# Kernel optimization log

Measured on AMD Instinct MI355X. Metric: run time of the kernel, lower is better.

Reference implementation:

```python
import jax, jax.numpy as jnp
import numpy as np

B, C, H, W = 8, 256, 64, 64
C8 = C // 8


def setup_inputs() -> dict:
    key = jax.random.key(0)
    ks = jax.random.split(key, 8)
    x = jax.random.normal(ks[0], (B, C, H, W), dtype=jnp.float32)
    # 1x1 convs == channel matmuls; store as [out_ch, in_ch] plus bias
    Wq = jax.random.normal(ks[1], (C8, C), dtype=jnp.float32) * (1.0 / np.sqrt(C))
    bq = jnp.zeros((C8,), dtype=jnp.float32)
    Wk = jax.random.normal(ks[2], (C8, C), dtype=jnp.float32) * (1.0 / np.sqrt(C))
    bk = jnp.zeros((C8,), dtype=jnp.float32)
    Wv = jax.random.normal(ks[3], (C, C), dtype=jnp.float32) * (1.0 / np.sqrt(C))
    bv = jnp.zeros((C,), dtype=jnp.float32)
    # gamma initialized to zero in the module, but use a nonzero value so the
    # attention branch actually contributes to the output being checked
    gamma = jnp.full((1,), 0.5, dtype=jnp.float32)
    return {"x": x, "Wq": Wq, "bq": bq, "Wk": Wk, "bk": bk, "Wv": Wv, "bv": bv, "gamma": gamma}


def reference(x, Wq, bq, Wk, bk, Wv, bv, gamma):
    b, c, h, w = x.shape
    n = h * w
    xf = x.reshape(b, c, n)                                  # [B, C, N]
    q = jnp.einsum('oc,bcn->bon', Wq, xf) + bq[None, :, None]  # [B, C8, N]
    k = jnp.einsum('oc,bcn->bon', Wk, xf) + bk[None, :, None]  # [B, C8, N]
    v = jnp.einsum('oc,bcn->bon', Wv, xf) + bv[None, :, None]  # [B, C,  N]
    # attention[b, i, j] = sum_d q[b, d, i] * k[b, d, j]  (no 1/sqrt(d) scaling!)
    scores = jnp.einsum('bdi,bdj->bij', q, k)                # [B, N, N]
    attn = jax.nn.softmax(scores, axis=-1)                   # softmax over j
    # out[b, c, i] = sum_j v[b, c, j] * attn[b, i, j]
    out = jnp.einsum('bcj,bij->bci', v, attn)                # [B, C, N]
    out = out.reshape(b, c, h, w)
    return gamma[0] * out + x
```

## Files before the change

### kernel.cpp

```cpp
#include <hip/hip_runtime.h>
#include <math.h>

#define BB 8
#define CC 256
#define NN 4096

typedef float f4 __attribute__((ext_vector_type(4)));
typedef short bh8 __attribute__((ext_vector_type(8)));

__device__ __forceinline__ unsigned short f2bf(float f) {
    unsigned u = __builtin_bit_cast(unsigned, f);
    u += 0x7fff + ((u >> 16) & 1);
    return (unsigned short)(u >> 16);
}

__global__ void prep_w_kernel(const float* __restrict__ Wq, const float* __restrict__ bq,
                              const float* __restrict__ Wk, const float* __restrict__ bk,
                              const float* __restrict__ Wv, const float* __restrict__ bv,
                              float* __restrict__ WcatT, float* __restrict__ bcat) {
    int idx = blockIdx.x * 256 + threadIdx.x;
    if (idx < 320) {
        bcat[idx] = (idx < 32) ? bq[idx] : (idx < 64 ? bk[idx - 32] : bv[idx - 64]);
    }
    if (idx < 320 * 256) {
        int o = idx >> 8;
        int c = idx & 255;
        float v = (o < 32) ? Wq[o * 256 + c]
                           : (o < 64 ? Wk[(o - 32) * 256 + c] : Wv[(o - 64) * 256 + c]);
        WcatT[c * 320 + o] = v;
    }
}

__global__ __launch_bounds__(256) void qkv_kernel(
    const float* __restrict__ x, const float* __restrict__ WcatT,
    const float* __restrict__ bcat,
    unsigned short* __restrict__ q64, unsigned short* __restrict__ k64,
    unsigned short* __restrict__ vC) {
    __shared__ float xs[256 * 64];
    __shared__ unsigned short qkl[64 * 128];
    unsigned short* vsl = (unsigned short*)xs;

    int blk = blockIdx.x;
    int b = blk >> 6;
    int i0 = (blk & 63) << 6;
    int t = threadIdx.x;

    const float* xb = x + ((size_t)b << 20);
    for (int idx = t; idx < 256 * 64; idx += 256) {
        int c = idx >> 6, ii = idx & 63;
        xs[idx] = xb[((size_t)c << 12) + i0 + ii];
    }
    __syncthreads();

    int to = t & 63;
    int tp = t >> 6;

    float acc[80];
#pragma unroll
    for (int uo = 0; uo < 5; ++uo) {
        float bias = bcat[to + 64 * uo];
#pragma unroll
        for (int pi = 0; pi < 16; ++pi) acc[uo * 16 + pi] = bias;
    }

    for (int c = 0; c < 256; ++c) {
        const float* wc = WcatT + c * 320 + to;
        float w0 = wc[0];
        float w1 = wc[64];
        float w2 = wc[128];
        float w3 = wc[192];
        float w4 = wc[256];
#pragma unroll
        for (int pi = 0; pi < 16; ++pi) {
            float xv = xs[c * 64 + tp + 4 * pi];
            acc[0 * 16 + pi] += w0 * xv;
            acc[1 * 16 + pi] += w1 * xv;
            acc[2 * 16 + pi] += w2 * xv;
            acc[3 * 16 + pi] += w3 * xv;
            acc[4 * 16 + pi] += w4 * xv;
        }
    }
    __syncthreads();

#pragma unroll
    for (int pi = 0; pi < 16; ++pi) {
        int ii = tp + 4 * pi;
        float v = acc[pi];
        unsigned short hi = f2bf(v);
        float vhi = __builtin_bit_cast(float, ((unsigned)hi) << 16);
        unsigned short lo = f2bf(v - vhi);
        if (to < 32) {
            qkl[ii * 128 + to] = hi;
            qkl[ii * 128 + 32 + to] = lo;
        } else {
            qkl[ii * 128 + 32 + to] = hi;
            qkl[ii * 128 + 64 + to] = lo;
        }
    }
#pragma unroll
    for (int uo = 1; uo < 5; ++uo) {
#pragma unroll
        for (int pi = 0; pi < 16; ++pi) {
            int c = to + 64 * (uo - 1);
            int ii = tp + 4 * pi;
            vsl[c * 66 + ii] = f2bf(acc[uo * 16 + pi]);
        }
    }
    __syncthreads();

    const unsigned* qk32 = (const unsigned*)qkl;
    unsigned* qb = (unsigned*)(q64 + ((size_t)(b * NN + i0)) * 64);
    unsigned* kb = (unsigned*)(k64 + ((size_t)(b * NN + i0)) * 64);
    for (int idx = t; idx < 64 * 32; idx += 256) {
        int row = idx >> 5, dw = idx & 31;
        qb[row * 32 + dw] = qk32[row * 64 + dw];
        kb[row * 32 + dw] = qk32[row * 64 + 32 + dw];
    }
    for (int idx = t; idx < 256 * 32; idx += 256) {
        int c = idx >> 5, dw = idx & 31;
        unsigned val = *(const unsigned*)(vsl + c * 66 + 2 * dw);
        *(unsigned*)(vC + ((size_t)(b * CC + c)) * NN + i0 + 2 * dw) = val;
    }
}

__global__ __launch_bounds__(256, 2) void attn_kernel(
    const unsigned short* __restrict__ q64, const unsigned short* __restrict__ k64,
    const unsigned short* __restrict__ vC, const float* __restrict__ x,
    const float* __restrict__ gamma, float* __restrict__ out) {
    __shared__ unsigned short vs[2][256 * 64];

    int t = threadIdx.x;
    int lane = t & 63;
    int w = t >> 6;
    int g = lane >> 4;
    int li = lane & 15;
    int blk = blockIdx.x;
    int b = blk & 7;
    int i0 = (blk >> 3) << 6;
    int qb = i0 + 16 * w;

    const unsigned short* vb = vC + ((size_t)b * CC) * NN;
    const unsigned short* kb = k64 + ((size_t)b * NN) * 64;

    bh8 qf[2];
#pragma unroll
    for (int s = 0; s < 2; ++s)
        qf[s] = *(const bh8*)(q64 + ((size_t)(b * NN + qb + li)) * 64 + s * 32 + 8 * g);

    f4 acc[16];
#pragma unroll
    for (int ct = 0; ct < 16; ++ct) acc[ct] = (f4){0.f, 0.f, 0.f, 0.f};
    float m = -INFINITY, l = 0.f;

    auto stageV = [&](int buf, int j0) {
#pragma unroll
        for (int s = 0; s < 8; ++s) {
            int c = 64 * w + 8 * s + (lane >> 3);
            int slot = (lane & 7) ^ (c & 7);
            const unsigned short* src = vb + (size_t)c * NN + j0 + slot * 8;
            __builtin_amdgcn_global_load_lds(
                (const __attribute__((address_space(1))) unsigned int*)src,
                (__attribute__((address_space(3))) unsigned int*)(&vs[buf][(64 * w + 8 * s) * 64]),
                16, 0, 0);
        }
    };
    auto loadK = [&](bh8 (&kf)[4][2], int j0) {
#pragma unroll
        for (int jt = 0; jt < 4; ++jt)
#pragma unroll
            for (int s = 0; s < 2; ++s)
                kf[jt][s] = *(const bh8*)(kb + (size_t)(j0 + 16 * jt + li) * 64 + s * 32 + 8 * g);
    };
    auto qkComp = [&](f4 (&sOut)[4], bh8 (&kc)[4][2]) {
#pragma unroll
        for (int jt = 0; jt < 4; ++jt) {
            f4 a = {0.f, 0.f, 0.f, 0.f};
            a = __builtin_amdgcn_mfma_f32_16x16x32_bf16(kc[jt][0], qf[0], a, 0, 0, 0);
            a = __builtin_amdgcn_mfma_f32_16x16x32_bf16(kc[jt][1], qf[0], a, 0, 0, 0);
            a = __builtin_amdgcn_mfma_f32_16x16x32_bf16(kc[jt][0], qf[1], a, 0, 0, 0);
            sOut[jt] = a;
        }
    };

    bh8 kf0[4][2], kf1[4][2];
    f4 sA[4], sB[4];

    stageV(0, 0);
    loadK(kf0, 0);
    loadK(kf1, 64);
    qkComp(sA, kf0);
    __syncthreads();

    auto step = [&](int tt, bh8 (&kNext)[4][2], bh8 (&kLoad)[4][2],
                    f4 (&sCur)[4], f4 (&sNxt)[4], int buf) {
        if (tt < 63) stageV(buf ^ 1, (tt + 1) << 6);
        if (tt < 62) loadK(kLoad, (tt + 2) << 6);

        if (tt < 63) qkComp(sNxt, kNext);

        float mx = sCur[0][0];
#pragma unroll
        for (int jt = 0; jt < 4; ++jt)
#pragma unroll
            for (int e = 0; e < 4; ++e) mx = fmaxf(mx, sCur[jt][e]);
        mx = fmaxf(mx, __shfl_xor(mx, 16));
        mx = fmaxf(mx, __shfl_xor(mx, 32));
        if (!__all(mx <= m + 8.f)) {
            float mnew = fmaxf(m, mx);
            float sc = __expf(m - mnew);
            l *= sc;
#pragma unroll
            for (int ct = 0; ct < 16; ++ct)
#pragma unroll
                for (int e = 0; e < 4; ++e) acc[ct][e] *= sc;
            m = mnew;
        }
        float sum = 0.f;
#pragma unroll
        for (int jt = 0; jt < 4; ++jt)
#pragma unroll
            for (int e = 0; e < 4; ++e) {
                float p = __expf(sCur[jt][e] - m);
                sCur[jt][e] = p;
                sum += p;
            }
        sum += __shfl_xor(sum, 16);
        sum += __shfl_xor(sum, 32);
        l += sum;

        const char* vsb = (const char*)vs[buf];
#pragma unroll
        for (int h = 0; h < 2; ++h) {
            bh8 pb;
            {
                unsigned pk[2][2];
#pragma unroll
                for (int tl = 0; tl < 2; ++tl)
#pragma unroll
                    for (int pp = 0; pp < 2; ++pp) {
                        unsigned lo16 = f2bf(sCur[2 * h + tl][2 * pp]);
                        unsigned hi16 = f2bf(sCur[2 * h + tl][2 * pp + 1]);
                        pk[tl][pp] = lo16 | (hi16 << 16);
                    }
                union { unsigned u[4]; bh8 v; } un;
#pragma unroll
                for (int d = 0; d < 4; ++d) {
                    int srcl = (((2 * g + (d >> 1)) & 3) << 4) | li;
                    unsigned a0 = (unsigned)__shfl((int)pk[0][d & 1], srcl);
                    unsigned a1 = (unsigned)__shfl((int)pk[1][d & 1], srcl);
                    un.u[d] = (g >> 1) ? a1 : a0;
                }
                pb = un.v;
            }
            __builtin_amdgcn_s_setprio(1);
#pragma unroll
            for (int ct = 0; ct < 16; ++ct) {
                int c = 16 * ct + li;
                int off = c * 128 + ((64 * h + 16 * g) ^ ((c & 7) << 4));
                bh8 vf = *(const bh8*)(vsb + off);
                acc[ct] = __builtin_amdgcn_mfma_f32_16x16x32_bf16(vf, pb, acc[ct], 0, 0, 0);
            }
            __builtin_amdgcn_s_setprio(0);
        }
        __syncthreads();
    };

    for (int tt = 0; tt < 64; tt += 2) {
        step(tt, kf1, kf0, sA, sB, 0);
        step(tt + 1, kf0, kf1, sB, sA, 1);
    }

    float gm = gamma[0];
    float rl = 1.f / l;
    const float* xb = x + ((size_t)b * CC) * NN;
    float* ob = out + ((size_t)b * CC) * NN;
    int i = qb + li;
#pragma unroll
    for (int ct = 0; ct < 16; ++ct)
#pragma unroll
        for (int e = 0; e < 4; ++e) {
            int c = 16 * ct + 4 * g + e;
            size_t idx = (size_t)c * NN + i;
            ob[idx] = gm * (acc[ct][e] * rl) + xb[idx];
        }
}

extern "C" void kernel_launch(void* const* d_in, const int* in_sizes, int n_in,
                              void* d_out, int out_size, void* d_ws, size_t ws_size,
                              hipStream_t stream) {
    const float* x = (const float*)d_in[0];
    const float* Wq = (const float*)d_in[1];
    const float* bq = (const float*)d_in[2];
    const float* Wk = (const float*)d_in[3];
    const float* bk = (const float*)d_in[4];
    const float* Wv = (const float*)d_in[5];
    const float* bv = (const float*)d_in[6];
    const float* gamma = (const float*)d_in[7];
    float* out = (float*)d_out;

    unsigned short* ws16 = (unsigned short*)d_ws;
    unsigned short* q64w = ws16;
    unsigned short* k64w = ws16 + 2097152;
    unsigned short* vCw = ws16 + 4194304;
    float* WcatT = (float*)((char*)d_ws + 25165824);
    float* bcat = WcatT + 81920;

    prep_w_kernel<<<320, 256, 0, stream>>>(Wq, bq, Wk, bk, Wv, bv, WcatT, bcat);
    qkv_kernel<<<BB * (NN / 64), 256, 0, stream>>>(x, WcatT, bcat, q64w, k64w, vCw);
    attn_kernel<<<512, 256, 0, stream>>>(q64w, k64w, vCw, x, gamma, out);
}
```

Before: 245.7 us.

## Prefetch V fragments into registers and vectorize QKV projection LDS reads

The attention step now loads the first half of the V tile fragments from shared memory at the start of each step, before the QK MFMAs and softmax. The PV product is restructured into interleaved load/MFMA batches so LDS reads overlap with matrix ops. The QKV projection kernel switches to float4 LDS reads by giving each thread 16 contiguous positions, and gets a launch bound of 2 blocks per CU. The cost is higher register pressure from holding 16 bh8 V fragments, which may cause spills or lower occupancy.

```diff
diff --git a/kernel.cpp b/kernel.cpp
--- a/kernel.cpp
+++ b/kernel.cpp
@@ -31,7 +31,7 @@
     }
 }
 
-__global__ __launch_bounds__(256) void qkv_kernel(
+__global__ __launch_bounds__(256, 2) void qkv_kernel(
     const float* __restrict__ x, const float* __restrict__ WcatT,
     const float* __restrict__ bcat,
     unsigned short* __restrict__ q64, unsigned short* __restrict__ k64,
@@ -70,21 +70,27 @@
         float w2 = wc[128];
         float w3 = wc[192];
         float w4 = wc[256];
-#pragma unroll
-        for (int pi = 0; pi < 16; ++pi) {
-            float xv = xs[c * 64 + tp + 4 * pi];
-            acc[0 * 16 + pi] += w0 * xv;
-            acc[1 * 16 + pi] += w1 * xv;
-            acc[2 * 16 + pi] += w2 * xv;
-            acc[3 * 16 + pi] += w3 * xv;
-            acc[4 * 16 + pi] += w4 * xv;
+        const float4* xr = (const float4*)(xs + c * 64 + 16 * tp);
+#pragma unroll
+        for (int q = 0; q < 4; ++q) {
+            float4 xv = xr[q];
+#pragma unroll
+            for (int e = 0; e < 4; ++e) {
+                int pi = 4 * q + e;
+                float xe = (e == 0) ? xv.x : (e == 1) ? xv.y : (e == 2) ? xv.z : xv.w;
+                acc[0 * 16 + pi] += w0 * xe;
+                acc[1 * 16 + pi] += w1 * xe;
+                acc[2 * 16 + pi] += w2 * xe;
+                acc[3 * 16 + pi] += w3 * xe;
+                acc[4 * 16 + pi] += w4 * xe;
+            }
         }
     }
     __syncthreads();
 
 #pragma unroll
     for (int pi = 0; pi < 16; ++pi) {
-        int ii = tp + 4 * pi;
+        int ii = 16 * tp + pi;
         float v = acc[pi];
         unsigned short hi = f2bf(v);
         float vhi = __builtin_bit_cast(float, ((unsigned)hi) << 16);
@@ -102,7 +108,7 @@
 #pragma unroll
         for (int pi = 0; pi < 16; ++pi) {
             int c = to + 64 * (uo - 1);
-            int ii = tp + 4 * pi;
+            int ii = 16 * tp + pi;
             vsl[c * 66 + ii] = f2bf(acc[uo * 16 + pi]);
         }
     }
@@ -181,6 +187,26 @@
             sOut[jt] = a;
         }
     };
+    auto mkpb = [&](f4 (&sCur)[4], int h) -> bh8 {
+        unsigned pk[2][2];
+#pragma unroll
+        for (int tl = 0; tl < 2; ++tl)
+#pragma unroll
+            for (int pp = 0; pp < 2; ++pp) {
+                unsigned lo16 = f2bf(sCur[2 * h + tl][2 * pp]);
+                unsigned hi16 = f2bf(sCur[2 * h + tl][2 * pp + 1]);
+                pk[tl][pp] = lo16 | (hi16 << 16);
+            }
+        union { unsigned u[4]; bh8 v; } un;
+#pragma unroll
+        for (int d = 0; d < 4; ++d) {
+            int srcl = (((2 * g + (d >> 1)) & 3) << 4) | li;
+            unsigned a0 = (unsigned)__shfl((int)pk[0][d & 1], srcl);
+            unsigned a1 = (unsigned)__shfl((int)pk[1][d & 1], srcl);
+            un.u[d] = (g >> 1) ? a1 : a0;
+        }
+        return un.v;
+    };
 
     bh8 kf0[4][2], kf1[4][2];
     f4 sA[4], sB[4];
@@ -191,8 +217,18 @@
     qkComp(sA, kf0);
     __syncthreads();
 
+    auto voff = [&](int ct, int h) {
+        return (16 * ct + li) * 128 + ((64 * h + 16 * g) ^ ((li & 7) << 4));
+    };
+
     auto step = [&](int tt, bh8 (&kNext)[4][2], bh8 (&kLoad)[4][2],
                     f4 (&sCur)[4], f4 (&sNxt)[4], int buf) {
+        const char* vsb = (const char*)vs[buf];
+
+        bh8 va[8], vb2[8];
+#pragma unroll
+        for (int ct = 0; ct < 8; ++ct) va[ct] = *(const bh8*)(vsb + voff(ct, 0));
+
         if (tt < 63) stageV(buf ^ 1, (tt + 1) << 6);
         if (tt < 62) loadK(kLoad, (tt + 2) << 6);
 
@@ -228,40 +264,29 @@
         sum += __shfl_xor(sum, 32);
         l += sum;
 
-        const char* vsb = (const char*)vs[buf];
-#pragma unroll
-        for (int h = 0; h < 2; ++h) {
-            bh8 pb;
-            {
-                unsigned pk[2][2];
-#pragma unroll
-                for (int tl = 0; tl < 2; ++tl)
-#pragma unroll
-                    for (int pp = 0; pp < 2; ++pp) {
-                        unsigned lo16 = f2bf(sCur[2 * h + tl][2 * pp]);
-                        unsigned hi16 = f2bf(sCur[2 * h + tl][2 * pp + 1]);
-                        pk[tl][pp] = lo16 | (hi16 << 16);
-                    }
-                union { unsigned u[4]; bh8 v; } un;
-#pragma unroll
-                for (int d = 0; d < 4; ++d) {
-                    int srcl = (((2 * g + (d >> 1)) & 3) << 4) | li;
-                    unsigned a0 = (unsigned)__shfl((int)pk[0][d & 1], srcl);
-                    unsigned a1 = (unsigned)__shfl((int)pk[1][d & 1], srcl);
-                    un.u[d] = (g >> 1) ? a1 : a0;
-                }
-                pb = un.v;
-            }
-            __builtin_amdgcn_s_setprio(1);
-#pragma unroll
-            for (int ct = 0; ct < 16; ++ct) {
-                int c = 16 * ct + li;
-                int off = c * 128 + ((64 * h + 16 * g) ^ ((c & 7) << 4));
-                bh8 vf = *(const bh8*)(vsb + off);
-                acc[ct] = __builtin_amdgcn_mfma_f32_16x16x32_bf16(vf, pb, acc[ct], 0, 0, 0);
-            }
-            __builtin_amdgcn_s_setprio(0);
-        }
+        bh8 pb0 = mkpb(sCur, 0);
+        bh8 pb1 = mkpb(sCur, 1);
+
+        __builtin_amdgcn_s_setprio(1);
+#pragma unroll
+        for (int ct = 0; ct < 8; ++ct) vb2[ct] = *(const bh8*)(vsb + voff(ct + 8, 0));
+#pragma unroll
+        for (int ct = 0; ct < 8; ++ct)
+            acc[ct] = __builtin_amdgcn_mfma_f32_16x16x32_bf16(va[ct], pb0, acc[ct], 0, 0, 0);
+#pragma unroll
+        for (int ct = 0; ct < 8; ++ct) va[ct] = *(const bh8*)(vsb + voff(ct, 1));
+#pragma unroll
+        for (int ct = 0; ct < 8; ++ct)
+            acc[ct + 8] = __builtin_amdgcn_mfma_f32_16x16x32_bf16(vb2[ct], pb0, acc[ct + 8], 0, 0, 0);
+#pragma unroll
+        for (int ct = 0; ct < 8; ++ct) vb2[ct] = *(const bh8*)(vsb + voff(ct + 8, 1));
+#pragma unroll
+        for (int ct = 0; ct < 8; ++ct)
+            acc[ct] = __builtin_amdgcn_mfma_f32_16x16x32_bf16(va[ct], pb1, acc[ct], 0, 0, 0);
+#pragma unroll
+        for (int ct = 0; ct < 8; ++ct)
+            acc[ct + 8] = __builtin_amdgcn_mfma_f32_16x16x32_bf16(vb2[ct], pb1, acc[ct + 8], 0, 0, 0);
+        __builtin_amdgcn_s_setprio(0);
         __syncthreads();
     };
 
```

Result: slower. 316.1 us (+28.7%).
